# Optimization experiments

Hardware: AMD Instinct MI355X
Metric: run time of the kernel (lower is better)

The kernel has to match this reference:

```python
import jax, jax.numpy as jnp
import numpy as np

N = 2_000_000
D = 128
B = 16

def setup_inputs() -> dict:
    key = jax.random.key(0)
    k1, k2 = jax.random.split(key)
    x = jax.random.normal(k1, (N, D), dtype=jnp.float32)
    batch = jnp.sort(jax.random.randint(k2, (N,), 0, B, dtype=jnp.int64))
    return {"x": x, "batch": batch, "num_segments": B}

def reference(x, batch, num_segments):
    # global_mean_pool: segment-mean of x over batch ids.
    sums = jax.ops.segment_sum(x, batch, num_segments=num_segments)  # [B, D]
    counts = jax.ops.segment_sum(jnp.ones((x.shape[0],), dtype=x.dtype), batch,
                                 num_segments=num_segments)          # [B]
    return sums / jnp.maximum(counts, 1.0)[:, None]
```

## Files before the change

kernel.cpp:

```cpp
#include <hip/hip_runtime.h>


#define D       128
#define D4      32
#define BSEG    16
#define BD      (BSEG * D)

#define MB_BLOCKS   512
#define MB_THREADS  1024
#define GSTRIDE     (MB_BLOCKS * MB_THREADS)

__global__ __launch_bounds__(256)
void boundary_kernel(const int* __restrict__ batch, int N, int* __restrict__ start)
{
    int t  = blockIdx.x * 256 + threadIdx.x;
    int i0 = t * 4;
    if (i0 >= N) return;

    int e[5];
    if (i0 + 4 <= N) {
        int4 b = *(const int4*)(batch + i0);
        e[0] = b.x; e[1] = b.y; e[2] = b.z; e[3] = b.w;
    } else {
        for (int k = 0; k < 4; ++k) e[k] = (i0 + k < N) ? batch[i0 + k] : batch[N - 1];
    }
    bool last = (i0 + 4 >= N);
    e[4] = last ? BSEG : batch[i0 + 4];

    if (i0 == 0) {
        int b0 = min(max(e[0], 0), BSEG - 1);
        for (int s = 0; s <= b0; ++s) start[s] = 0;
    }
    for (int k = 0; k < 4; ++k) {
        int a = min(max(e[k], 0), BSEG - 1);
        int b = (k == 3) ? (last ? BSEG : min(max(e[4], 0), BSEG - 1))
                         : min(max(e[k + 1], 0), BSEG - 1);
        int pos = i0 + k + 1; if (pos > N) pos = N;
        for (int s = a + 1; s <= b; ++s) start[s] = pos;
    }
}

__global__ __launch_bounds__(MB_THREADS, 8)
void pool_main(const float4* __restrict__ x4, const int* __restrict__ start,
               float* __restrict__ partial )
{
    __shared__ float lds_sum[BSEG][D];
    __shared__ int   lds_st[BSEG + 1];

    const int tid = threadIdx.x;
    for (int i = tid; i < BD; i += MB_THREADS) ((float*)lds_sum)[i] = 0.0f;
    if (tid <= BSEG) lds_st[tid] = start[tid];
    __syncthreads();

    const int gtid = blockIdx.x * MB_THREADS + tid;
    const int col4 = tid & (D4 - 1);
    const int lane = tid & 63;

    #pragma unroll 1
    for (int s = 0; s < BSEG; ++s) {
        const int i0 = lds_st[s] * D4 + gtid;
        const int e1 = lds_st[s + 1] * D4;
        float4 a = make_float4(0.f, 0.f, 0.f, 0.f);
        for (int i = i0; i < e1; i += GSTRIDE) {
            float4 v = x4[i];
            a.x += v.x; a.y += v.y; a.z += v.z; a.w += v.w;
        }
        a.x += __shfl_down(a.x, 32);
        a.y += __shfl_down(a.y, 32);
        a.z += __shfl_down(a.z, 32);
        a.w += __shfl_down(a.w, 32);
        if (lane < 32) {
            atomicAdd(&lds_sum[s][col4 * 4 + 0], a.x);
            atomicAdd(&lds_sum[s][col4 * 4 + 1], a.y);
            atomicAdd(&lds_sum[s][col4 * 4 + 2], a.z);
            atomicAdd(&lds_sum[s][col4 * 4 + 3], a.w);
        }
    }
    __syncthreads();

    if (tid < BD / 4) {
        float4* pp = (float4*)(partial + (long)blockIdx.x * BD);
        pp[tid] = ((const float4*)lds_sum)[tid];
    }
}

__global__ __launch_bounds__(256)
void stage2_kernel(const float* __restrict__ partial, float* __restrict__ sums)
{
    int g   = blockIdx.x * 256 + threadIdx.x;
    int col = g & (BD - 1);
    int grp = g >> 11;
    const int rows = MB_BLOCKS / 16;
    int r0 = grp * rows;
    float s = 0.f;
    for (int k = 0; k < rows; ++k)
        s += partial[(r0 + k) * BD + col];
    atomicAdd(&sums[col], s);
}

__global__ __launch_bounds__(256)
void div_kernel(const float* __restrict__ sums, const int* __restrict__ start,
                float* __restrict__ out)
{
    int i = blockIdx.x * 256 + threadIdx.x;
    if (i < BD) {
        int s = i >> 7;
        float c = (float)(start[s + 1] - start[s]);
        out[i] = sums[i] / fmaxf(c, 1.0f);
    }
}

__global__ __launch_bounds__(256)
void pool_sum_fb(const float* __restrict__ x, const int* __restrict__ batch,
                 float* __restrict__ sums, float* __restrict__ counts,
                 int N, int nblocks)
{
    __shared__ float lds_sum[BSEG][D];
    __shared__ float lds_cnt[BSEG];
    const int tid = threadIdx.x;
    for (int i = tid; i < BD; i += 256) ((float*)lds_sum)[i] = 0.0f;
    if (tid < BSEG) lds_cnt[tid] = 0.0f;
    __syncthreads();

    const int chunk = (N + nblocks - 1) / nblocks;
    const int r0 = blockIdx.x * chunk;
    int r1 = r0 + chunk; if (r1 > N) r1 = N;
    const int col4 = tid & (D4 - 1);
    const int rlane = tid >> 5;
    const float4* x4 = (const float4*)x;

    float4 acc = make_float4(0.f, 0.f, 0.f, 0.f);
    int cnt = 0, cur = -1;
    for (int r = r0 + rlane; r < r1; r += 8) {
        int seg = batch[r];
        if (seg != cur) {
            if (cur >= 0) {
                atomicAdd(&lds_sum[cur][col4 * 4 + 0], acc.x);
                atomicAdd(&lds_sum[cur][col4 * 4 + 1], acc.y);
                atomicAdd(&lds_sum[cur][col4 * 4 + 2], acc.z);
                atomicAdd(&lds_sum[cur][col4 * 4 + 3], acc.w);
                if (col4 == 0) atomicAdd(&lds_cnt[cur], (float)cnt);
            }
            acc = make_float4(0.f, 0.f, 0.f, 0.f); cnt = 0;
            cur = (seg >= 0 && seg < BSEG) ? seg : -1;
        }
        if (cur >= 0) {
            float4 v = x4[(long)r * D4 + col4];
            acc.x += v.x; acc.y += v.y; acc.z += v.z; acc.w += v.w; cnt++;
        }
    }
    if (cur >= 0) {
        atomicAdd(&lds_sum[cur][col4 * 4 + 0], acc.x);
        atomicAdd(&lds_sum[cur][col4 * 4 + 1], acc.y);
        atomicAdd(&lds_sum[cur][col4 * 4 + 2], acc.z);
        atomicAdd(&lds_sum[cur][col4 * 4 + 3], acc.w);
        if (col4 == 0) atomicAdd(&lds_cnt[cur], (float)cnt);
    }
    __syncthreads();
    for (int i = tid; i < BD; i += 256) {
        float v = ((float*)lds_sum)[i];
        if (v != 0.0f) atomicAdd(&sums[i], v);
    }
    if (tid < BSEG) {
        float c = lds_cnt[tid];
        if (c != 0.0f) atomicAdd(&counts[tid], c);
    }
}

__global__ __launch_bounds__(256)
void div_fb(const float* __restrict__ sums, const float* __restrict__ counts,
            float* __restrict__ out)
{
    int i = blockIdx.x * 256 + threadIdx.x;
    if (i < BD) out[i] = sums[i] / fmaxf(counts[i >> 7], 1.0f);
}

extern "C" void kernel_launch(void* const* d_in, const int* in_sizes, int n_in,
                              void* d_out, int out_size, void* d_ws, size_t ws_size,
                              hipStream_t stream)
{
    const float* x     = (const float*)d_in[0];
    const int*   batch = (const int*)d_in[1];
    const int    N     = in_sizes[1];

    int*   start   = (int*)d_ws;
    float* sums    = (float*)d_ws + 32;
    float* partial = (float*)d_ws + 32 + BD;
    const size_t need = (size_t)(32 + BD + (size_t)MB_BLOCKS * BD) * sizeof(float);

    if (ws_size >= need) {
        hipMemsetAsync(sums, 0, BD * sizeof(float), stream);
        boundary_kernel<<<(N / 4 + 255) / 256, 256, 0, stream>>>(batch, N, start);
        pool_main<<<MB_BLOCKS, MB_THREADS, 0, stream>>>((const float4*)x, start, partial);
        stage2_kernel<<<128, 256, 0, stream>>>(partial, sums);
        div_kernel<<<8, 256, 0, stream>>>(sums, start, (float*)d_out);
    } else {
        float* fsums   = (float*)d_ws;
        float* fcounts = fsums + BD;
        hipMemsetAsync(d_ws, 0, (BD + BSEG) * sizeof(float), stream);
        pool_sum_fb<<<2048, 256, 0, stream>>>(x, batch, fsums, fcounts, N, 2048);
        div_fb<<<8, 256, 0, stream>>>(fsums, fcounts, (float*)d_out);
    }
}
```

Measured before the change: 193.9 us.

## Fuse memset and divide into neighbouring kernels, unroll main load loop by two

Zeroing of the sums buffer moves from a separate memset into block 0 of the boundary kernel. The divide kernel is folded into the stage-2 reduction: a last-block-done atomic counter lets the final block compute the means. The main accumulation loop now issues two independent float4 loads per iteration into separate accumulators to raise memory-level parallelism. Together these drop two launches and add a threadfence/atomic handshake at the end of stage 2.

```diff
diff --git a/kernel.cpp b/kernel.cpp
--- a/kernel.cpp
+++ b/kernel.cpp
@@ -11,8 +11,15 @@
 #define GSTRIDE     (MB_BLOCKS * MB_THREADS)
 
 __global__ __launch_bounds__(256)
-void boundary_kernel(const int* __restrict__ batch, int N, int* __restrict__ start)
-{
+void boundary_kernel(const int* __restrict__ batch, int N,
+                     int* __restrict__ start, float* __restrict__ sums,
+                     int* __restrict__ done)
+{
+    if (blockIdx.x == 0) {
+        for (int i = threadIdx.x; i < BD; i += 256) sums[i] = 0.0f;
+        if (threadIdx.x == 0) *done = 0;
+    }
+
     int t  = blockIdx.x * 256 + threadIdx.x;
     int i0 = t * 4;
     if (i0 >= N) return;
@@ -58,22 +65,31 @@
 
     #pragma unroll 1
     for (int s = 0; s < BSEG; ++s) {
-        const int i0 = lds_st[s] * D4 + gtid;
+        int i = lds_st[s] * D4 + gtid;
         const int e1 = lds_st[s + 1] * D4;
-        float4 a = make_float4(0.f, 0.f, 0.f, 0.f);
-        for (int i = i0; i < e1; i += GSTRIDE) {
+        float4 a0 = make_float4(0.f, 0.f, 0.f, 0.f);
+        float4 a1 = a0;
+        for (; i + GSTRIDE < e1; i += 2 * GSTRIDE) {
+            float4 v0 = x4[i];
+            float4 v1 = x4[i + GSTRIDE];
+            a0.x += v0.x; a0.y += v0.y; a0.z += v0.z; a0.w += v0.w;
+            a1.x += v1.x; a1.y += v1.y; a1.z += v1.z; a1.w += v1.w;
+        }
+        if (i < e1) {
             float4 v = x4[i];
-            a.x += v.x; a.y += v.y; a.z += v.z; a.w += v.w;
-        }
-        a.x += __shfl_down(a.x, 32);
-        a.y += __shfl_down(a.y, 32);
-        a.z += __shfl_down(a.z, 32);
-        a.w += __shfl_down(a.w, 32);
+            a0.x += v.x; a0.y += v.y; a0.z += v.z; a0.w += v.w;
+        }
+        a0.x += a1.x; a0.y += a1.y; a0.z += a1.z; a0.w += a1.w;
+
+        a0.x += __shfl_down(a0.x, 32);
+        a0.y += __shfl_down(a0.y, 32);
+        a0.z += __shfl_down(a0.z, 32);
+        a0.w += __shfl_down(a0.w, 32);
         if (lane < 32) {
-            atomicAdd(&lds_sum[s][col4 * 4 + 0], a.x);
-            atomicAdd(&lds_sum[s][col4 * 4 + 1], a.y);
-            atomicAdd(&lds_sum[s][col4 * 4 + 2], a.z);
-            atomicAdd(&lds_sum[s][col4 * 4 + 3], a.w);
+            atomicAdd(&lds_sum[s][col4 * 4 + 0], a0.x);
+            atomicAdd(&lds_sum[s][col4 * 4 + 1], a0.y);
+            atomicAdd(&lds_sum[s][col4 * 4 + 2], a0.z);
+            atomicAdd(&lds_sum[s][col4 * 4 + 3], a0.w);
         }
     }
     __syncthreads();
@@ -85,8 +101,11 @@
 }
 
 __global__ __launch_bounds__(256)
-void stage2_kernel(const float* __restrict__ partial, float* __restrict__ sums)
-{
+void stage2_div(const float* __restrict__ partial, const int* __restrict__ start,
+                float* __restrict__ sums, int* __restrict__ done,
+                float* __restrict__ out)
+{
+    __shared__ bool is_last;
     int g   = blockIdx.x * 256 + threadIdx.x;
     int col = g & (BD - 1);
     int grp = g >> 11;
@@ -96,17 +115,23 @@
     for (int k = 0; k < rows; ++k)
         s += partial[(r0 + k) * BD + col];
     atomicAdd(&sums[col], s);
-}
-
-__global__ __launch_bounds__(256)
-void div_kernel(const float* __restrict__ sums, const int* __restrict__ start,
-                float* __restrict__ out)
-{
-    int i = blockIdx.x * 256 + threadIdx.x;
-    if (i < BD) {
-        int s = i >> 7;
-        float c = (float)(start[s + 1] - start[s]);
-        out[i] = sums[i] / fmaxf(c, 1.0f);
+
+    __threadfence();
+    __syncthreads();
+    if (threadIdx.x == 0) {
+        int t = atomicAdd(done, 1);
+        is_last = (t == gridDim.x - 1);
+    }
+    __syncthreads();
+    if (is_last) {
+        __threadfence();
+        for (int i = threadIdx.x; i < BD; i += 256) {
+            float v = __hip_atomic_load(&sums[i], __ATOMIC_ACQUIRE,
+                                        __HIP_MEMORY_SCOPE_AGENT);
+            int seg = i >> 7;
+            float c = (float)(start[seg + 1] - start[seg]);
+            out[i] = v / fmaxf(c, 1.0f);
+        }
     }
 }
 
@@ -184,16 +209,15 @@
     const int    N     = in_sizes[1];
 
     int*   start   = (int*)d_ws;
+    int*   done    = (int*)d_ws + 24;
     float* sums    = (float*)d_ws + 32;
     float* partial = (float*)d_ws + 32 + BD;
     const size_t need = (size_t)(32 + BD + (size_t)MB_BLOCKS * BD) * sizeof(float);
 
     if (ws_size >= need) {
-        hipMemsetAsync(sums, 0, BD * sizeof(float), stream);
-        boundary_kernel<<<(N / 4 + 255) / 256, 256, 0, stream>>>(batch, N, start);
+        boundary_kernel<<<(N / 4 + 255) / 256, 256, 0, stream>>>(batch, N, start, sums, done);
         pool_main<<<MB_BLOCKS, MB_THREADS, 0, stream>>>((const float4*)x, start, partial);
-        stage2_kernel<<<128, 256, 0, stream>>>(partial, sums);
-        div_kernel<<<8, 256, 0, stream>>>(sums, start, (float*)d_out);
+        stage2_div<<<128, 256, 0, stream>>>(partial, start, sums, done, (float*)d_out);
     } else {
         float* fsums   = (float*)d_ws;
         float* fcounts = fsums + BD;
```

Result: slower. 212.0 us (+9.3%).
